# Kernel optimization log

Measured on AMD Instinct MI355X. Metric: run time of the kernel, lower is better.

Reference implementation:

```python
import jax, jax.numpy as jnp
import numpy as np

G = 4096   # num_genes
P = 4096   # num_perts
H = 64     # hidden_size
B = 4      # num_graphs
E1 = 81920 # coexpress edges
E2 = 81920 # GO edges
FF = 512   # transformer ffn
NH = 2     # attention heads
INTER, LAT = 32, 16  # VAE dims

def _bn(x, g, b, eps=1e-5):
    # BatchNorm1d in training mode: batch stats (biased var)
    m = x.mean(0); v = x.var(0)
    return (x - m) / jnp.sqrt(v + eps) * g + b

def _ln(x, g, b, eps=1e-5):
    m = x.mean(-1, keepdims=True); v = x.var(-1, keepdims=True)
    return (x - m) / jnp.sqrt(v + eps) * g + b

def _mlp2(x, w1, b1, g1, be1, w2, b2, g2, be2):
    # MLP([a,b,c]) builds Linear->BN->ReLU->Linear->BN (trailing ReLU stripped)
    h = jax.nn.relu(_bn(x @ w1.T + b1, g1, be1))
    return _bn(h @ w2.T + b2, g2, be2)

def _sgconv(x, ei, ew, w, b, n):
    # SGConv K=1: gcn_norm (self loops, symmetric norm) then linear
    src = jnp.concatenate([ei[0], jnp.arange(n)])
    dst = jnp.concatenate([ei[1], jnp.arange(n)])
    wgt = jnp.concatenate([ew, jnp.ones((n,), ew.dtype)])
    deg = jax.ops.segment_sum(wgt, dst, num_segments=n)
    dinv = jnp.where(deg > 0, 1.0 / jnp.sqrt(jnp.where(deg > 0, deg, 1.0)), 0.0)
    norm = dinv[dst] * wgt * dinv[src]
    agg = jax.ops.segment_sum(norm[:, None] * x[src], dst, num_segments=n)
    return agg @ w.T + b

def setup_inputs():
    ks = iter(jax.random.split(jax.random.key(0), 80))
    def nrm(shape, s=0.05):
        return jax.random.normal(next(ks), shape, dtype=jnp.float32) * s
    d = {}
    d['x'] = jax.random.uniform(next(ks), (B * G,), dtype=jnp.float32)
    d['pert_idx'] = jax.random.randint(next(ks), (B, 2), 0, P)
    d['mask'] = jnp.zeros((G, G), jnp.float32)
    d['ei_co'] = jax.random.randint(next(ks), (2, E1), 0, G)
    d['w_co'] = jax.random.uniform(next(ks), (E1,), dtype=jnp.float32)
    d['ei_go'] = jax.random.randint(next(ks), (2, E2), 0, P)
    d['w_go'] = jax.random.uniform(next(ks), (E2,), dtype=jnp.float32)
    d['gene_emb'] = nrm((G, H)); d['emb_pos'] = nrm((G, H)); d['pert_tbl'] = nrm((P, H))
    d['sg_co_w'] = nrm((H, H)); d['sg_co_b'] = jnp.zeros((H,))
    d['sg_go_w'] = nrm((H, H)); d['sg_go_b'] = jnp.zeros((H,))
    d['bn_emb_g'] = jnp.ones((H,)); d['bn_emb_b'] = jnp.zeros((H,))
    for pre, din, dout in [('etv2_1', H, H), ('etv2_2', H, H), ('pf_1', H, H), ('pf_2', H, H), ('rw_1', H, 2 * H), ('rw_2', 2 * H, H)]:
        d[pre + '_w'] = nrm((dout, din)); d[pre + '_b'] = jnp.zeros((dout,))
        d[pre + '_g'] = jnp.ones((dout,)); d[pre + '_be'] = jnp.zeros((dout,))
    d['bnpb_g'] = jnp.ones((H,)); d['bnpb_b'] = jnp.zeros((H,))
    d['attn_in_w'] = nrm((3 * H, H)); d['attn_in_b'] = jnp.zeros((3 * H,))
    d['attn_out_w'] = nrm((H, H)); d['attn_out_b'] = jnp.zeros((H,))
    d['ln1_g'] = jnp.ones((H,)); d['ln1_b'] = jnp.zeros((H,))
    d['ff1_w'] = nrm((FF, H)); d['ff1_b'] = jnp.zeros((FF,))
    d['ff2_w'] = nrm((H, FF)); d['ff2_b'] = jnp.zeros((H,))
    d['ln2_g'] = jnp.ones((H,)); d['ln2_b'] = jnp.zeros((H,))
    d['indv_w1'] = nrm((G, H)); d['indv_b1'] = jnp.zeros((G,))
    d['vae_e1_w'] = nrm((INTER, G)); d['vae_e1_b'] = jnp.zeros((INTER,))
    d['vae_mu_w'] = nrm((LAT, INTER)); d['vae_mu_b'] = jnp.zeros((LAT,))
    d['vae_lv_w'] = nrm((LAT, INTER)); d['vae_lv_b'] = jnp.zeros((LAT,))
    d['vae_d1_w'] = nrm((INTER, LAT)); d['vae_d1_b'] = jnp.zeros((INTER,))
    d['vae_d2_w'] = nrm((G, INTER)); d['vae_d2_b'] = jnp.zeros((G,))
    d['eps'] = jax.random.normal(next(ks), (B, LAT), dtype=jnp.float32)
    return d

def reference(x, pert_idx, mask, ei_co, w_co, ei_go, w_go, gene_emb, emb_pos, pert_tbl, sg_co_w, sg_co_b, sg_go_w, sg_go_b, bn_emb_g, bn_emb_b, etv2_1_w, etv2_1_b, etv2_1_g, etv2_1_be, etv2_2_w, etv2_2_b, etv2_2_g, etv2_2_be, pf_1_w, pf_1_b, pf_1_g, pf_1_be, pf_2_w, pf_2_b, pf_2_g, pf_2_be, rw_1_w, rw_1_b, rw_1_g, rw_1_be, rw_2_w, rw_2_b, rw_2_g, rw_2_be, bnpb_g, bnpb_b, attn_in_w, attn_in_b, attn_out_w, attn_out_b, ln1_g, ln1_b, ff1_w, ff1_b, ff2_w, ff2_b, ln2_g, ln2_b, indv_w1, indv_b1, vae_e1_w, vae_e1_b, vae_mu_w, vae_mu_b, vae_lv_w, vae_lv_b, vae_d1_w, vae_d1_b, vae_d2_w, vae_d2_b, eps):
    # gene base embedding (identical across graphs until pert fusion)
    base = jax.nn.relu(_bn(gene_emb, bn_emb_g, bn_emb_b))               # [G,H]
    pos = _sgconv(emb_pos, ei_co, w_co, sg_co_w, sg_co_b, G)            # 1 gene-GNN layer
    base = base + 0.2 * pos
    base = _mlp2(base, etv2_1_w, etv2_1_b, etv2_1_g, etv2_1_be, etv2_2_w, etv2_2_b, etv2_2_g, etv2_2_be)
    # pert embeddings propagated on GO graph
    pge = _sgconv(pert_tbl, ei_go, w_go, sg_go_w, sg_go_b, P)           # [P,H]
    # per-graph pert_track: sum of pert embeddings (all pert_idx valid)
    psum = pge[pert_idx].sum(axis=1)                                    # [B,H]
    etot = _mlp2(psum, pf_1_w, pf_1_b, pf_1_g, pf_1_be, pf_2_w, pf_2_b, pf_2_g, pf_2_be)
    base_b = base[None, :, :] + etot[:, None, :]                        # [B,G,H]
    flat = jax.nn.relu(_bn(base_b.reshape(B * G, H), bnpb_g, bnpb_b))
    out = _mlp2(flat, rw_1_w, rw_1_b, rw_1_g, rw_1_be, rw_2_w, rw_2_b, rw_2_g, rw_2_be)
    out = out.reshape(B, G, H)
    # transformer encoder layer (post-norm, relu, nhead=2), eval/no-dropout
    qkv = out @ attn_in_w.T + attn_in_b
    q, k, v = jnp.split(qkv, 3, axis=-1)
    hd = H // NH
    q = q.reshape(B, G, NH, hd); k = k.reshape(B, G, NH, hd); v = v.reshape(B, G, NH, hd)
    sc = jnp.einsum('bqhd,bkhd->bhqk', q, k) / np.float32(np.sqrt(hd)) + mask
    a = jax.nn.softmax(sc, axis=-1)
    ctx = jnp.einsum('bhqk,bkhd->bqhd', a, v).reshape(B, G, H)
    att = ctx @ attn_out_w.T + attn_out_b
    h1 = _ln(out + att, ln1_g, ln1_b)
    ff = jax.nn.relu(h1 @ ff1_w.T + ff1_b) @ ff2_w.T + ff2_b
    enc = _ln(h1 + ff, ln2_g, ln2_b)
    # per-gene linear: (enc.unsqueeze(-1)*indv_w1).sum(2)+indv_b1
    pred0 = jnp.einsum('bgh,gh->bg', enc, indv_w1) + indv_b1
    # VAE branch on raw expression
    xr = x.reshape(B, G)
    he = jax.nn.relu(xr @ vae_e1_w.T + vae_e1_b)
    mu = he @ vae_mu_w.T + vae_mu_b
    lv = he @ vae_lv_w.T + vae_lv_b
    z = mu + eps * jnp.exp(0.5 * lv)
    hdc = jax.nn.relu(z @ vae_d1_w.T + vae_d1_b)
    recon = hdc @ vae_d2_w.T + vae_d2_b
    kl = -0.5 * jnp.mean(jnp.sum(1.0 + lv - mu ** 2 - jnp.exp(lv), axis=1))
    recon = jnp.where(xr == 0, 0.0, recon)
    pred = pred0 + recon
    return (pred, kl)
```

## Files before the change

### kernel.cpp

```cpp
#include <hip/hip_runtime.h>
#include <hip/hip_bf16.h>
#include <math.h>

#define GG 4096
#define PP 4096
#define HH 64
#define BB 4
#define E1N 81920
#define E2N 81920
#define FFD 512
#define BNEPS 1e-5f
#define LOG2E 1.44269504088896341f
#define QPRE (0.17677669529663687f * LOG2E)

typedef unsigned short ushort_t;
typedef unsigned int uint_t;
using sh8 = __attribute__((ext_vector_type(8))) short;
using sh4 = __attribute__((ext_vector_type(4))) short;
using f4  = __attribute__((ext_vector_type(4))) float;

#if __has_builtin(__builtin_amdgcn_mfma_f32_16x16x16bf16_1k)
#define MFMA16(a, b, c) __builtin_amdgcn_mfma_f32_16x16x16bf16_1k((a), (b), (c), 0, 0, 0)
#elif __has_builtin(__builtin_amdgcn_mfma_f32_16x16x16_bf16)
#define MFMA16(a, b, c) __builtin_amdgcn_mfma_f32_16x16x16_bf16((a), (b), (c), 0, 0, 0)
#else
static __device__ inline f4 mfma16_asm(sh4 a, sh4 b, f4 c) {
    f4 d;
    asm volatile("v_mfma_f32_16x16x16_bf16 %0, %1, %2, %3"
                 : "=v"(d) : "v"(a), "v"(b), "v"(c));
    return d;
}
#define MFMA16(a, b, c) mfma16_asm((a), (b), (c))
#endif

#define OF_STATS   0
#define OF_DEGCO   2048
#define OF_DEGGO   6144
#define OF_PSLOT   10240
#define OF_ETOT    10752
#define OF_HDC     11008
#define OF_HE      11136
#define OF_AGGCO   12288
#define OF_BASEIN  274432
#define OF_Y1      536576
#define OF_Y2      798720
#define OF_FLAT    1060864
#define OF_RW1     2109440
#define OF_RW2     4206592
#define OF_OUT     5255168
#define OF_QKV     6303744
#define OF_H1      10498048
#define OF_QB      OF_AGGCO
#define OF_KB      (OF_AGGCO + 524288)
#define OF_VF      OF_FLAT
#define OF_OPA     OF_QKV
#define OF_OPB     OF_OUT
#define OF_LP      OF_RW1
#define OPS        1048576
#define OF_W1B     9449472
#define OF_W2B     9465856
#define OF_H1B     9482240
#define OF_FFT     OF_FLAT

__device__ inline ushort_t f2b(float f) {
    uint_t u = __builtin_bit_cast(uint_t, f);
    u += 0x7FFFu + ((u >> 16) & 1u);
    return (ushort_t)(u >> 16);
}

__device__ inline void gld16(const void* gptr, void* lptr) {
    __builtin_amdgcn_global_load_lds(
        (const __attribute__((address_space(1))) uint_t*)gptr,
        (__attribute__((address_space(3))) uint_t*)lptr, 16, 0, 0);
}

__device__ void dev_vae_he(int bid, const float* __restrict__ x, const float* __restrict__ W,
                           const float* __restrict__ bias, float* he, float* sh) {
    int b = bid >> 5, i = bid & 31;
    float s = 0.f;
    for (int g = threadIdx.x; g < 4096; g += 256) s += x[b * 4096 + g] * W[i * 4096 + g];
    sh[threadIdx.x] = s;
    __syncthreads();
    for (int o = 128; o > 0; o >>= 1) {
        if (threadIdx.x < o) sh[threadIdx.x] += sh[threadIdx.x + o];
        __syncthreads();
    }
    if (threadIdx.x == 0) he[b * 32 + i] = fmaxf(sh[0] + bias[i], 0.f);
}

__device__ void dev_vae_mid(const float* __restrict__ he,
                            const float* __restrict__ muw, const float* __restrict__ mub,
                            const float* __restrict__ lvw, const float* __restrict__ lvb,
                            const float* __restrict__ d1w, const float* __restrict__ d1b,
                            const float* __restrict__ eps, float* hdc, float* klout, float* zs) {
    int t = threadIdx.x;
    if (t < 64) {
        int b = t >> 4, l = t & 15;
        float mu = mub[l], lv = lvb[l];
        for (int i = 0; i < 32; i++) {
            float hv = he[b * 32 + i];
            mu += hv * muw[l * 32 + i];
            lv += hv * lvw[l * 32 + i];
        }
        zs[t] = mu + eps[t] * expf(0.5f * lv);
        float kterm = 1.f + lv - mu * mu - expf(lv);
        for (int o = 32; o > 0; o >>= 1) kterm += __shfl_xor(kterm, o, 64);
        if (t == 0) klout[0] = -0.5f * kterm * 0.25f;
    }
    __syncthreads();
    if (t < 128) {
        int b = t >> 5, i = t & 31;
        float a = d1b[i];
        for (int l = 0; l < 16; l++) a += zs[b * 16 + l] * d1w[i * 16 + l];
        hdc[t] = fmaxf(a, 0.f);
    }
}

__device__ void dev_edge_deg(int bid, const int* __restrict__ ei, const float* __restrict__ w,
                             float* deg, int E) {
    int e = bid * 256 + threadIdx.x;
    if (e < E) atomicAdd(&deg[ei[E + e]], w[e]);
}

__device__ void dev_cs_part(int bid, const float* __restrict__ X, int N,
                            float* sum, float* sumsq, float* sh) {
    int t = threadIdx.x;
    int col = t & 63, ro = t >> 6;
    int rows = N >> 8;
    int r0 = bid * rows;
    float s = 0.f, q = 0.f;
    for (int r = r0 + ro; r < r0 + rows; r += 4) {
        float v = X[r * 64 + col];
        s += v; q += v * v;
    }
    float* ls = sh; float* lq = sh + 256;
    ls[t] = s; lq[t] = q;
    __syncthreads();
    if (t < 64) {
        for (int j = t + 64; j < 256; j += 64) { s += ls[j]; q += lq[j]; }
        atomicAdd(&sum[t], s);
        atomicAdd(&sumsq[t], q);
    }
}

__device__ void dev_edge_agg(int bid, const int* __restrict__ ei, const float* __restrict__ w,
                             const float* __restrict__ deg, const float* __restrict__ x,
                             float* agg) {
    int gid = bid * 256 + threadIdx.x;
    int e = gid >> 6, h = gid & 63;
    if (e < E1N) {
        int src = ei[e], dst = ei[E1N + e];
        float norm = rsqrtf(deg[dst]) * w[e] * rsqrtf(deg[src]);
        atomicAdd(&agg[dst * HH + h], norm * x[src * HH + h]);
    }
}

__device__ void dev_pert_edges(int bid, const int* __restrict__ pidx, const int* __restrict__ ei,
                               const float* __restrict__ w, const float* __restrict__ deg,
                               const float* __restrict__ tbl, float* pslot) {
    int e = bid * 256 + threadIdx.x;
    if (e >= E2N) return;
    int dst = ei[E2N + e];
    int src = ei[e];
    for (int s = 0; s < 8; s++) {
        if (pidx[s] == dst) {
            float norm = rsqrtf(deg[dst]) * w[e] * rsqrtf(deg[src]);
            for (int h = 0; h < 64; h++)
                atomicAdd(&pslot[s * 64 + h], norm * tbl[src * 64 + h]);
        }
    }
}

__device__ void dev_base_combine(int bid, const float* __restrict__ gene_emb,
                                 const float* __restrict__ agg, const float* __restrict__ emb_pos,
                                 const float* __restrict__ deg,
                                 const float* __restrict__ W, const float* __restrict__ bias,
                                 const float* __restrict__ bsum, const float* __restrict__ bsq,
                                 const float* __restrict__ bg, const float* __restrict__ bb,
                                 float* out, float* sh) {
    float* Wt = sh;
    float* a = sh + 4160;
    int t = threadIdx.x;
    for (int i = t; i < 4096; i += 256) Wt[(i & 63) * 65 + (i >> 6)] = W[i];
    int rr = t >> 6, h = t & 63;
    int g = bid * 4 + rr;
    a[rr * 64 + h] = agg[g * 64 + h] + emb_pos[g * 64 + h] / deg[g];
    __syncthreads();
    float y = bias[h];
    const float* ar = a + rr * 64;
    #pragma unroll 8
    for (int k = 0; k < 64; k++) y += ar[k] * Wt[k * 65 + h];
    const float invN = 1.0f / (float)GG;
    float m = bsum[h] * invN;
    float is_ = rsqrtf(bsq[h] * invN - m * m + BNEPS);
    float v = gene_emb[g * 64 + h];
    v = (v - m) * is_ * bg[h] + bb[h];
    v = fmaxf(v, 0.f);
    out[g * 64 + h] = v + 0.2f * y;
}

__device__ void dev_pert_mlp(const float* __restrict__ pslot, const int* __restrict__ pidx,
                             const float* __restrict__ deg, const float* __restrict__ tbl,
                             const float* __restrict__ gw, const float* __restrict__ gb,
                             const float* __restrict__ w1, const float* __restrict__ b1,
                             const float* __restrict__ g1, const float* __restrict__ be1,
                             const float* __restrict__ w2, const float* __restrict__ b2,
                             const float* __restrict__ g2, const float* __restrict__ be2,
                             float* etot, float* sh) {
    float* pge = sh;
    float* psum = sh + 512;
    float* y = sh + 768;
    float* mh = sh + 1024;
    float* ih = sh + 1088;
    int t = threadIdx.x;
    for (int j = t; j < 512; j += 256) {
        int s = j >> 6, h = j & 63;
        int n = pidx[s];
        float invd = 1.0f / deg[n];
        float acc = gb[h];
        for (int k = 0; k < 64; k++)
            acc += (pslot[s * 64 + k] + tbl[n * 64 + k] * invd) * gw[h * 64 + k];
        pge[j] = acc;
    }
    __syncthreads();
    { int b = t >> 6, h = t & 63; psum[t] = pge[2 * b * 64 + h] + pge[(2 * b + 1) * 64 + h]; }
    __syncthreads();
    { int h = t & 63; int b = t >> 6;
      float acc = b1[h];
      for (int k = 0; k < 64; k++) acc += psum[b * 64 + k] * w1[h * 64 + k];
      y[t] = acc; }
    __syncthreads();
    if (t < 64) {
        float s = 0.f, sq = 0.f;
        for (int b = 0; b < 4; b++) { float v = y[b * 64 + t]; s += v; sq += v * v; }
        float m = s * 0.25f;
        mh[t] = m; ih[t] = rsqrtf(sq * 0.25f - m * m + BNEPS);
    }
    __syncthreads();
    { int h = t & 63;
      float v = (y[t] - mh[h]) * ih[h] * g1[h] + be1[h];
      psum[t] = fmaxf(v, 0.f); }
    __syncthreads();
    { int h = t & 63; int b = t >> 6;
      float acc = b2[h];
      for (int k = 0; k < 64; k++) acc += psum[b * 64 + k] * w2[h * 64 + k];
      y[t] = acc; }
    __syncthreads();
    if (t < 64) {
        float s = 0.f, sq = 0.f;
        for (int b = 0; b < 4; b++) { float v = y[b * 64 + t]; s += v; sq += v * v; }
        float m = s * 0.25f;
        mh[t] = m; ih[t] = rsqrtf(sq * 0.25f - m * m + BNEPS);
    }
    __syncthreads();
    { int h = t & 63;
      etot[t] = (y[t] - mh[h]) * ih[h] * g2[h] + be2[h]; }
}

__global__ void k_fat1(float* ws, const float* __restrict__ x,
                       const float* __restrict__ ve1_w, const float* __restrict__ ve1_b,
                       const float* __restrict__ ff1_w, const float* __restrict__ ff2_w) {
    __shared__ float sh[256];
    int bid = blockIdx.x;
    if (bid < 1024) {
        ws[OF_AGGCO + bid * 256 + threadIdx.x] = 0.f;
    } else if (bid < 1034) {
        int i = (bid - 1024) * 256 + threadIdx.x;
        if (i < 2048) ws[OF_STATS + i] = 0.f;
        else if (i < 2560) ws[OF_PSLOT + (i - 2048)] = 0.f;
    } else if (bid < 1066) {
        ws[OF_DEGCO + (bid - 1034) * 256 + threadIdx.x] = 1.0f;
    } else if (bid < 1194) {
        dev_vae_he(bid - 1066, x, ve1_w, ve1_b, ws + OF_HE, sh);
    } else {
        int i = (bid - 1194) * 256 + threadIdx.x;
        ushort_t* W1b = (ushort_t*)(ws + OF_W1B);
        ushort_t* W2b = (ushort_t*)(ws + OF_W2B);
        if (i < 32768) W1b[i] = f2b(ff1_w[i]);
        else W2b[i - 32768] = f2b(ff2_w[i - 32768]);
    }
}

__global__ void k_fat2(float* ws, const int* __restrict__ ei_co, const float* __restrict__ w_co,
                       const int* __restrict__ ei_go, const float* __restrict__ w_go,
                       const float* __restrict__ gene_emb,
                       const float* __restrict__ vmu_w, const float* __restrict__ vmu_b,
                       const float* __restrict__ vlv_w, const float* __restrict__ vlv_b,
                       const float* __restrict__ vd1_w, const float* __restrict__ vd1_b,
                       const float* __restrict__ veps, float* klout) {
    __shared__ float sh[512];
    int bid = blockIdx.x;
    if (bid < 320) dev_edge_deg(bid, ei_co, w_co, ws + OF_DEGCO, E1N);
    else if (bid < 640) dev_edge_deg(bid - 320, ei_go, w_go, ws + OF_DEGGO, E2N);
    else if (bid < 896) dev_cs_part(bid - 640, gene_emb, GG, ws + OF_STATS, ws + OF_STATS + 128, sh);
    else dev_vae_mid(ws + OF_HE, vmu_w, vmu_b, vlv_w, vlv_b, vd1_w, vd1_b, veps,
                     ws + OF_HDC, klout, sh);
}

__global__ void k_fat3(float* ws, const int* __restrict__ ei_co, const float* __restrict__ w_co,
                       const float* __restrict__ emb_pos, const int* __restrict__ pidx,
                       const int* __restrict__ ei_go, const float* __restrict__ w_go,
                       const float* __restrict__ pert_tbl) {
    int bid = blockIdx.x;
    if (bid < 20480) dev_edge_agg(bid, ei_co, w_co, ws + OF_DEGCO, emb_pos, ws + OF_AGGCO);
    else dev_pert_edges(bid - 20480, pidx, ei_go, w_go, ws + OF_DEGGO, pert_tbl, ws + OF_PSLOT);
}

__global__ void k_fat4(float* ws, const float* __restrict__ gene_emb,
                       const float* __restrict__ emb_pos,
                       const float* __restrict__ sg_co_w, const float* __restrict__ sg_co_b,
                       const float* __restrict__ bn_emb_g, const float* __restrict__ bn_emb_b,
                       const int* __restrict__ pidx, const float* __restrict__ pert_tbl,
                       const float* __restrict__ gw, const float* __restrict__ gb,
                       const float* __restrict__ w1, const float* __restrict__ b1,
                       const float* __restrict__ g1, const float* __restrict__ be1,
                       const float* __restrict__ w2, const float* __restrict__ b2,
                       const float* __restrict__ g2, const float* __restrict__ be2) {
    __shared__ float sh[4416];
    int bid = blockIdx.x;
    if (bid < 1024)
        dev_base_combine(bid, gene_emb, ws + OF_AGGCO, emb_pos, ws + OF_DEGCO,
                         sg_co_w, sg_co_b, ws + OF_STATS, ws + OF_STATS + 128,
                         bn_emb_g, bn_emb_b, ws + OF_BASEIN, sh);
    else
        dev_pert_mlp(ws + OF_PSLOT, pidx, ws + OF_DEGGO, pert_tbl, gw, gb,
                     w1, b1, g1, be1, w2, b2, g2, be2, ws + OF_ETOT, sh);
}

__launch_bounds__(256)
__global__ void k_gemm64(const float* __restrict__ X, const float* __restrict__ W,
                         const float* __restrict__ bias, float* __restrict__ Y,
                         int Cin, int Cout,
                         const float* __restrict__ bnsum, const float* __restrict__ bnsq,
                         const float* __restrict__ bng, const float* __restrict__ bnb,
                         float invN, int relu_in,
                         float* __restrict__ outsum, float* __restrict__ outsq) {
    __shared__ float Xs[64][66];
    __shared__ float Ws[64][66];
    __shared__ float bsc[64], bsh[64];
    const int t = threadIdx.x;
    const int row0 = blockIdx.x * 64, cb = blockIdx.y * 64;
    const int tx = t & 15, ty = t >> 4;
    const int c0 = tx * 4, r0 = ty * 4;
    float acc[4][4];
    #pragma unroll
    for (int j = 0; j < 4; j++)
        #pragma unroll
        for (int i = 0; i < 4; i++) acc[j][i] = 0.f;

    for (int k0 = 0; k0 < Cin; k0 += 64) {
        __syncthreads();
        if (t < 64) {
            float sc = 1.f, sh = 0.f;
            if (bnsum) {
                int c = k0 + t;
                float m = bnsum[c] * invN;
                float is_ = rsqrtf(bnsq[c] * invN - m * m + BNEPS);
                sc = is_ * bng[c]; sh = bnb[c] - m * sc;
            }
            bsc[t] = sc; bsh[t] = sh;
        }
        __syncthreads();
        for (int i = t; i < 1024; i += 256) {
            int r = i >> 4, kq = (i & 15) * 4;
            float4 v = *(const float4*)&X[(size_t)(row0 + r) * Cin + k0 + kq];
            float e0 = v.x * bsc[kq] + bsh[kq];
            float e1 = v.y * bsc[kq + 1] + bsh[kq + 1];
            float e2 = v.z * bsc[kq + 2] + bsh[kq + 2];
            float e3 = v.w * bsc[kq + 3] + bsh[kq + 3];
            if (relu_in) {
                e0 = fmaxf(e0, 0.f); e1 = fmaxf(e1, 0.f);
                e2 = fmaxf(e2, 0.f); e3 = fmaxf(e3, 0.f);
            }
            Xs[r][kq] = e0; Xs[r][kq + 1] = e1; Xs[r][kq + 2] = e2; Xs[r][kq + 3] = e3;
            float4 wv = *(const float4*)&W[(size_t)(cb + r) * Cin + k0 + kq];
            Ws[r][kq] = wv.x; Ws[r][kq + 1] = wv.y; Ws[r][kq + 2] = wv.z; Ws[r][kq + 3] = wv.w;
        }
        __syncthreads();
        #pragma unroll 4
        for (int k = 0; k < 64; k += 2) {
            float2 a[4], b[4];
            #pragma unroll
            for (int j = 0; j < 4; j++) a[j] = *(const float2*)&Xs[r0 + j][k];
            #pragma unroll
            for (int i = 0; i < 4; i++) b[i] = *(const float2*)&Ws[c0 + i][k];
            #pragma unroll
            for (int j = 0; j < 4; j++)
                #pragma unroll
                for (int i = 0; i < 4; i++)
                    acc[j][i] += a[j].x * b[i].x + a[j].y * b[i].y;
        }
    }
    float4 bi = *(const float4*)&bias[cb + c0];
    float scol[4] = {0.f, 0.f, 0.f, 0.f}, qcol[4] = {0.f, 0.f, 0.f, 0.f};
    #pragma unroll
    for (int j = 0; j < 4; j++) {
        float4 o;
        o.x = acc[j][0] + bi.x; o.y = acc[j][1] + bi.y;
        o.z = acc[j][2] + bi.z; o.w = acc[j][3] + bi.w;
        *(float4*)&Y[(size_t)(row0 + r0 + j) * Cout + cb + c0] = o;
        scol[0] += o.x; scol[1] += o.y; scol[2] += o.z; scol[3] += o.w;
        qcol[0] += o.x * o.x; qcol[1] += o.y * o.y;
        qcol[2] += o.z * o.z; qcol[3] += o.w * o.w;
    }
    if (outsum) {
        __syncthreads();
        #pragma unroll
        for (int i = 0; i < 4; i++) { Xs[ty][c0 + i] = scol[i]; Ws[ty][c0 + i] = qcol[i]; }
        __syncthreads();
        if (t < 64) {
            float ss = 0.f, qq = 0.f;
            #pragma unroll
            for (int r = 0; r < 16; r++) { ss += Xs[r][t]; qq += Ws[r][t]; }
            atomicAdd(&outsum[cb + t], ss);
            atomicAdd(&outsq[cb + t], qq);
        }
    }
}

__launch_bounds__(256)
__global__ void k_gemm_qkv(const float* __restrict__ X, const float* __restrict__ W,
                           const float* __restrict__ bias,
                           const float* __restrict__ bnsum, const float* __restrict__ bnsq,
                           const float* __restrict__ bng, const float* __restrict__ bnb,
                           ushort_t* __restrict__ Qb, ushort_t* __restrict__ Kb,
                           ushort_t* __restrict__ Vf) {
    __shared__ float Xs[64][66];
    __shared__ float Ws[64][66];
    __shared__ float bsc[64], bsh[64];
    const int t = threadIdx.x;
    const int row0 = blockIdx.x * 64, yb = blockIdx.y, cb = yb * 64;
    const int tx = t & 15, ty = t >> 4;
    const int c0 = tx * 4, r0 = ty * 4;
    const float invN = 1.0f / (float)(BB * GG);
    if (t < 64) {
        float m = bnsum[t] * invN;
        float is_ = rsqrtf(bnsq[t] * invN - m * m + BNEPS);
        float sc = is_ * bng[t];
        bsc[t] = sc; bsh[t] = bnb[t] - m * sc;
    }
    __syncthreads();
    for (int i = t; i < 1024; i += 256) {
        int r = i >> 4, kq = (i & 15) * 4;
        float4 v = *(const float4*)&X[(size_t)(row0 + r) * 64 + kq];
        Xs[r][kq] = v.x * bsc[kq] + bsh[kq];
        Xs[r][kq + 1] = v.y * bsc[kq + 1] + bsh[kq + 1];
        Xs[r][kq + 2] = v.z * bsc[kq + 2] + bsh[kq + 2];
        Xs[r][kq + 3] = v.w * bsc[kq + 3] + bsh[kq + 3];
        float4 wv = *(const float4*)&W[(size_t)(cb + r) * 64 + kq];
        Ws[r][kq] = wv.x; Ws[r][kq + 1] = wv.y; Ws[r][kq + 2] = wv.z; Ws[r][kq + 3] = wv.w;
    }
    __syncthreads();
    float acc[4][4];
    #pragma unroll
    for (int j = 0; j < 4; j++)
        #pragma unroll
        for (int i = 0; i < 4; i++) acc[j][i] = 0.f;
    #pragma unroll 4
    for (int k = 0; k < 64; k += 2) {
        float2 a[4], b[4];
        #pragma unroll
        for (int j = 0; j < 4; j++) a[j] = *(const float2*)&Xs[r0 + j][k];
        #pragma unroll
        for (int i = 0; i < 4; i++) b[i] = *(const float2*)&Ws[c0 + i][k];
        #pragma unroll
        for (int j = 0; j < 4; j++)
            #pragma unroll
            for (int i = 0; i < 4; i++)
                acc[j][i] += a[j].x * b[i].x + a[j].y * b[i].y;
    }
    float4 bi = *(const float4*)&bias[cb + c0];
    const int b2 = row0 >> 12, tile = (row0 & 4095) >> 6;
    if (yb < 2) {
        ushort_t* Dst = (yb == 0) ? Qb : Kb;
        const float sc2 = (yb == 0) ? QPRE : 1.0f;
        const int h = c0 >> 5, d = c0 & 31;
        #pragma unroll
        for (int j = 0; j < 4; j++) {
            union { ushort_t u[4]; uint2 v; } pk;
            pk.u[0] = f2b((acc[j][0] + bi.x) * sc2);
            pk.u[1] = f2b((acc[j][1] + bi.y) * sc2);
            pk.u[2] = f2b((acc[j][2] + bi.z) * sc2);
            pk.u[3] = f2b((acc[j][3] + bi.w) * sc2);
            int g = (row0 & 4095) + r0 + j;
            *(uint2*)&Dst[((size_t)(b2 * 2 + h) * GG + g) * 32 + d] = pk.v;
        }
    } else {
        __syncthreads();
        #pragma unroll
        for (int j = 0; j < 4; j++) {
            Xs[r0 + j][c0] = acc[j][0] + bi.x;
            Xs[r0 + j][c0 + 1] = acc[j][1] + bi.y;
            Xs[r0 + j][c0 + 2] = acc[j][2] + bi.z;
            Xs[r0 + j][c0 + 3] = acc[j][3] + bi.w;
        }
        __syncthreads();
        #pragma unroll
        for (int h = 0; h < 2; h++) {
            union { ushort_t u[8]; uint4 v; } pk;
            #pragma unroll
            for (int j = 0; j < 8; j++) {
                int idx = t * 8 + j;
                int g2 = idx >> 8, L = (idx >> 2) & 63, i = idx & 3;
                int key = (g2 >> 1) * 16 + ((L >> 4) << 2) + i;
                int d = ((g2 & 1) << 4) + (L & 15);
                pk.u[j] = f2b(Xs[key][h * 32 + d]);
            }
            *(uint4*)&Vf[((size_t)((b2 * 2 + h) * 64 + tile)) * 2048 + t * 8] = pk.v;
        }
    }
}

__global__ void k_flatpre(const float* __restrict__ y2, const float* __restrict__ etot,
                          const float* __restrict__ bsum, const float* __restrict__ bsq,
                          const float* __restrict__ g2, const float* __restrict__ b2,
                          float* __restrict__ out,
                          float* __restrict__ osum, float* __restrict__ osq) {
    int t = threadIdx.x;
    int h = t & 63, ro = t >> 6;
    int row0 = blockIdx.x * 64;
    const float invN = 1.0f / (float)GG;
    float m = bsum[h] * invN;
    float is_ = rsqrtf(bsq[h] * invN - m * m + BNEPS);
    float sc = is_ * g2[h];
    float sh = b2[h] - m * sc;
    float s = 0.f, q = 0.f;
    for (int r = row0 + ro; r < row0 + 64; r += 4) {
        int b = r >> 12, gh = (r & 4095) * 64 + h;
        float v = y2[gh] * sc + sh + etot[b * 64 + h];
        out[r * 64 + h] = v;
        s += v; q += v * v;
    }
    __shared__ float ls[256], lq[256];
    ls[t] = s; lq[t] = q;
    __syncthreads();
    if (t < 64) {
        s = ls[t] + ls[t + 64] + ls[t + 128] + ls[t + 192];
        q = lq[t] + lq[t + 64] + lq[t + 128] + lq[t + 192];
        atomicAdd(&osum[t], s);
        atomicAdd(&osq[t], q);
    }
}

__launch_bounds__(256)
__global__ void k_attn_mfma(const ushort_t* __restrict__ Qb, const ushort_t* __restrict__ Kb,
                            const ushort_t* __restrict__ Vf, const float* __restrict__ mask,
                            float* __restrict__ opA, float* __restrict__ opB,
                            float* __restrict__ Lp) {
    __shared__ ushort_t Kl[2][4096];
    __shared__ ushort_t Vl[2][4096];
    const int bh = blockIdx.y;
    const int split = blockIdx.z;
    const int q0 = blockIdx.x * 64;
    const int kstart = split * (GG / 4), kend = kstart + (GG / 4);
    const int t = threadIdx.x;
    const int lane = t & 63, w = t >> 6;
    const int l15 = lane & 15, quad = lane >> 4;

    const sh8 qf = *(const sh8*)&Qb[((size_t)bh * GG + q0 + w * 16 + l15) * 32 + quad * 8];
    const float* mrow = mask + (size_t)(q0 + w * 16 + l15) * GG + quad * 4;

    const size_t kfth = ((size_t)bh * GG + (t >> 6) * 16 + (t & 15)) * 32 + ((t >> 4) & 3) * 8;
    const size_t vfbh = (size_t)bh * 64;

    gld16(Kb + kfth + (size_t)kstart * 32, &Kl[0][t * 8]);
    gld16(Kb + kfth + (size_t)(kstart + 64) * 32, &Kl[0][2048 + t * 8]);
    gld16(Vf + (vfbh + (kstart >> 6)) * 2048 + t * 8, &Vl[0][t * 8]);
    gld16(Vf + (vfbh + (kstart >> 6) + 1) * 2048 + t * 8, &Vl[0][2048 + t * 8]);

    f4 O0 = {0.f, 0.f, 0.f, 0.f}, O1 = {0.f, 0.f, 0.f, 0.f};
    float ls = 0.f;

    for (int k0 = kstart; k0 < kend; k0 += 128) {
        const int cur = ((k0 - kstart) >> 7) & 1;
        __syncthreads();
        if (k0 + 128 < kend) {
            const int nxt = cur ^ 1;
            gld16(Kb + kfth + (size_t)(k0 + 128) * 32, &Kl[nxt][t * 8]);
            gld16(Kb + kfth + (size_t)(k0 + 192) * 32, &Kl[nxt][2048 + t * 8]);
            gld16(Vf + (vfbh + ((k0 + 128) >> 6)) * 2048 + t * 8, &Vl[nxt][t * 8]);
            gld16(Vf + (vfbh + ((k0 + 128) >> 6) + 1) * 2048 + t * 8, &Vl[nxt][2048 + t * 8]);
        }
        #pragma unroll
        for (int half = 0; half < 2; half++) {
            const ushort_t* Kh = &Kl[cur][half * 2048];
            const ushort_t* Vh = &Vl[cur][half * 2048];
            const int kk = k0 + half * 64;
            float4 mv[4];
            #pragma unroll
            for (int i2 = 0; i2 < 4; i2++) mv[i2] = *(const float4*)&mrow[kk + i2 * 16];
            f4 s[4];
            #pragma unroll
            for (int i2 = 0; i2 < 4; i2++) {
                sh8 kf = *(const sh8*)&Kh[(i2 * 64 + lane) * 8];
                f4 z = {0.f, 0.f, 0.f, 0.f};
                s[i2] = __builtin_amdgcn_mfma_f32_16x16x32_bf16(kf, qf, z, 0, 0, 0);
            }
            #pragma unroll
            for (int i2 = 0; i2 < 4; i2++) {
                float p0 = exp2f(fmaf(mv[i2].x, LOG2E, s[i2][0]));
                float p1 = exp2f(fmaf(mv[i2].y, LOG2E, s[i2][1]));
                float p2 = exp2f(fmaf(mv[i2].z, LOG2E, s[i2][2]));
                float p3 = exp2f(fmaf(mv[i2].w, LOG2E, s[i2][3]));
                ls += (p0 + p1) + (p2 + p3);
                union { __hip_bfloat162 h2[2]; sh4 v; } pkp;
                pkp.h2[0] = __float22bfloat162_rn(float2{p0, p1});
                pkp.h2[1] = __float22bfloat162_rn(float2{p2, p3});
                sh4 vf0 = *(const sh4*)&Vh[((i2 * 2 + 0) * 64 + lane) * 4];
                sh4 vf1 = *(const sh4*)&Vh[((i2 * 2 + 1) * 64 + lane) * 4];
                O0 = MFMA16(pkp.v, vf0, O0);
                O1 = MFMA16(pkp.v, vf1, O1);
            }
        }
    }
    ls += __shfl_xor(ls, 16, 64);
    ls += __shfl_xor(ls, 32, 64);
    float* op = (split < 3) ? (opA + (size_t)split * OPS) : opB;
    #pragma unroll
    for (int r = 0; r < 4; r++) {
        int q = q0 + w * 16 + quad * 4 + r;
        size_t o = ((size_t)bh * GG + q) * 32 + l15;
        op[o] = O0[r];
        op[o + 16] = O1[r];
    }
    if (quad == 0)
        Lp[split * 32768 + bh * GG + q0 + w * 16 + l15] = ls;
}

__global__ void k_attn_out_ln(const float* __restrict__ opA, const float* __restrict__ opB,
                              const float* __restrict__ Lp, const float* __restrict__ yrw2,
                              const float* __restrict__ W, const float* __restrict__ bias,
                              const float* __restrict__ bsum, const float* __restrict__ bsq,
                              const float* __restrict__ bg, const float* __restrict__ bb,
                              const float* __restrict__ lg, const float* __restrict__ lb,
                              float* __restrict__ h1, ushort_t* __restrict__ h1b) {
    __shared__ float Wt[64][65];
    __shared__ float Cs[16][65];
    __shared__ ushort_t Hs[16][64];
    int t = threadIdx.x;
    int row0 = blockIdx.x * 16;
    for (int i = t; i < 4096; i += 256) Wt[i & 63][i >> 6] = W[i];
    {
        int col = t & 63, rl = t >> 6;
        int hh = col >> 5, d = col & 31;
        #pragma unroll
        for (int jj = 0; jj < 4; jj++) {
            int row = row0 + rl + jj * 4;
            int b = row >> 12, q = row & 4095;
            int bhq = (b * 2 + hh) * GG + q;
            size_t oi = (size_t)bhq * 32 + d;
            float num = opA[oi] + opA[OPS + oi] + opA[2 * OPS + oi] + opB[oi];
            float den = Lp[bhq] + Lp[32768 + bhq] + Lp[65536 + bhq] + Lp[98304 + bhq];
            Cs[rl + jj * 4][col] = num / den;
        }
    }
    __syncthreads();
    int rr = t >> 6, lane = t & 63;
    const float invN = 1.0f / (float)(BB * GG);
    float m = bsum[lane] * invN;
    float is_ = rsqrtf(bsq[lane] * invN - m * m + BNEPS);
    #pragma unroll
    for (int j = 0; j < 4; j++) {
        int lrow = rr * 4 + j;
        int row = row0 + lrow;
        float acc = bias[lane];
        const float* cr = Cs[lrow];
        #pragma unroll 8
        for (int k = 0; k < 64; k++) acc += cr[k] * Wt[k][lane];
        float ov = (yrw2[row * 64 + lane] - m) * is_ * bg[lane] + bb[lane];
        float v = ov + acc;
        float s = v;
        for (int o = 32; o > 0; o >>= 1) s += __shfl_xor(s, o, 64);
        float mean = s * (1.f / 64.f);
        float d = v - mean;
        float sq = d * d;
        for (int o = 32; o > 0; o >>= 1) sq += __shfl_xor(sq, o, 64);
        float inv = rsqrtf(sq * (1.f / 64.f) + BNEPS);
        float hv = d * inv * lg[lane] + lb[lane];
        h1[row * 64 + lane] = hv;
        Hs[lrow][lane] = f2b(hv);
    }
    __syncthreads();
    if (t < 128) {
        int kt = t >> 6, lane6 = t & 63;
        int q2 = (lane6 >> 4) & 3, r15 = lane6 & 15;
        union { ushort_t u[8]; uint4 v; } pk;
        #pragma unroll
        for (int j = 0; j < 8; j++) pk.u[j] = Hs[r15][kt * 32 + q2 * 8 + j];
        *(uint4*)&h1b[((size_t)blockIdx.x * 2 + kt) * 512 + lane6 * 8] = pk.v;
    }
}

__launch_bounds__(256)
__global__ void k_ffn1(const ushort_t* __restrict__ h1b, const ushort_t* __restrict__ W1b,
                       const float* __restrict__ b1, ushort_t* __restrict__ fft) {
    __shared__ ushort_t Xl[4096];
    __shared__ ushort_t Wl[4096];
    const int t = threadIdx.x;
    const int rowblock = blockIdx.x, colblock = blockIdx.y;
    const int cb = colblock * 64;
    const int lane = t & 63, w = t >> 6;
    const int l15 = lane & 15, quad = lane >> 4;
    #pragma unroll
    for (int kt = 0; kt < 2; kt++) {
        gld16(h1b + (size_t)(((rowblock * 4 + w) * 2 + kt) * 512 + lane * 8),
              &Xl[(w * 2 + kt) * 512 + lane * 8]);
        gld16(W1b + (size_t)((cb + w * 16 + l15) * 64 + kt * 32 + quad * 8),
              &Wl[(w * 2 + kt) * 512 + lane * 8]);
    }
    __syncthreads();
    sh8 xf0 = *(const sh8*)&Xl[(w * 2 + 0) * 512 + lane * 8];
    sh8 xf1 = *(const sh8*)&Xl[(w * 2 + 1) * 512 + lane * 8];
    #pragma unroll
    for (int c = 0; c < 4; c++) {
        sh8 wf0 = *(const sh8*)&Wl[(c * 2 + 0) * 512 + lane * 8];
        sh8 wf1 = *(const sh8*)&Wl[(c * 2 + 1) * 512 + lane * 8];
        f4 z = {0.f, 0.f, 0.f, 0.f};
        f4 acc = __builtin_amdgcn_mfma_f32_16x16x32_bf16(wf0, xf0, z, 0, 0, 0);
        acc = __builtin_amdgcn_mfma_f32_16x16x32_bf16(wf1, xf1, acc, 0, 0, 0);
        float4 bv = *(const float4*)&b1[cb + c * 16 + quad * 4];
        union { ushort_t u[4]; uint2 v; } pk;
        pk.u[0] = f2b(fmaxf(acc[0] + bv.x, 0.f));
        pk.u[1] = f2b(fmaxf(acc[1] + bv.y, 0.f));
        pk.u[2] = f2b(fmaxf(acc[2] + bv.z, 0.f));
        pk.u[3] = f2b(fmaxf(acc[3] + bv.w, 0.f));
        int kt512 = colblock * 2 + (c >> 1);
        int quadp = (c & 1) * 2 + (quad >> 1);
        int j0 = (quad & 1) * 4;
        size_t o = ((size_t)(((rowblock * 4 + w) * 16 + kt512) * 64 + quadp * 16 + l15)) * 8 + j0;
        *(uint2*)&fft[o] = pk.v;
    }
}

__launch_bounds__(256)
__global__ void k_ffn2(const ushort_t* __restrict__ fft, const ushort_t* __restrict__ W2b,
                       const float* __restrict__ b2, const float* __restrict__ h1,
                       const float* __restrict__ lg, const float* __restrict__ lb,
                       const float* __restrict__ indvw, const float* __restrict__ indvb,
                       const float* __restrict__ hdc, const float* __restrict__ d2w,
                       const float* __restrict__ d2b, const float* __restrict__ x,
                       float* __restrict__ outp) {
    __shared__ ushort_t Xl[2][4096];
    __shared__ ushort_t Wl[2][4096];
    const int t = threadIdx.x;
    const int rowblock = blockIdx.x;
    const int lane = t & 63, w = t >> 6;
    const int l15 = lane & 15, quad = lane >> 4;

    #pragma unroll
    for (int kt = 0; kt < 2; kt++) {
        gld16(fft + (size_t)((((rowblock * 4 + w) * 16) + kt) * 64 + lane) * 8,
              &Xl[0][(w * 2 + kt) * 512 + lane * 8]);
        gld16(W2b + (size_t)((w * 16 + l15) * 512 + kt * 32 + quad * 8),
              &Wl[0][(w * 2 + kt) * 512 + lane * 8]);
    }
    f4 acc[4];
    #pragma unroll
    for (int c = 0; c < 4; c++) acc[c] = f4{0.f, 0.f, 0.f, 0.f};

    for (int k0 = 0; k0 < 512; k0 += 64) {
        const int cur = (k0 >> 6) & 1;
        __syncthreads();
        if (k0 + 64 < 512) {
            const int nxt = cur ^ 1;
            const int ktb = (k0 + 64) >> 5;
            #pragma unroll
            for (int kt = 0; kt < 2; kt++) {
                gld16(fft + (size_t)((((rowblock * 4 + w) * 16) + ktb + kt) * 64 + lane) * 8,
                      &Xl[nxt][(w * 2 + kt) * 512 + lane * 8]);
                gld16(W2b + (size_t)((w * 16 + l15) * 512 + k0 + 64 + kt * 32 + quad * 8),
                      &Wl[nxt][(w * 2 + kt) * 512 + lane * 8]);
            }
        }
        #pragma unroll
        for (int kt = 0; kt < 2; kt++) {
            sh8 xf = *(const sh8*)&Xl[cur][(w * 2 + kt) * 512 + lane * 8];
            #pragma unroll
            for (int c = 0; c < 4; c++) {
                sh8 wf = *(const sh8*)&Wl[cur][(c * 2 + kt) * 512 + lane * 8];
                acc[c] = __builtin_amdgcn_mfma_f32_16x16x32_bf16(wf, xf, acc[c], 0, 0, 0);
            }
        }
    }
    const int row = rowblock * 64 + w * 16 + l15;
    const int b = row >> 12, g = row & 4095;
    float v[4][4];
    float s = 0.f, sq = 0.f;
    #pragma unroll
    for (int c = 0; c < 4; c++) {
        float4 bv = *(const float4*)&b2[c * 16 + quad * 4];
        float4 hv = *(const float4*)&h1[(size_t)row * 64 + c * 16 + quad * 4];
        v[c][0] = hv.x + acc[c][0] + bv.x;
        v[c][1] = hv.y + acc[c][1] + bv.y;
        v[c][2] = hv.z + acc[c][2] + bv.z;
        v[c][3] = hv.w + acc[c][3] + bv.w;
        #pragma unroll
        for (int i = 0; i < 4; i++) { s += v[c][i]; sq += v[c][i] * v[c][i]; }
    }
    s += __shfl_xor(s, 16, 64);  s += __shfl_xor(s, 32, 64);
    sq += __shfl_xor(sq, 16, 64); sq += __shfl_xor(sq, 32, 64);
    float mean = s * (1.f / 64.f);
    float inv = rsqrtf(sq * (1.f / 64.f) - mean * mean + BNEPS);
    float pd = 0.f;
    #pragma unroll
    for (int c = 0; c < 4; c++) {
        float4 lgv = *(const float4*)&lg[c * 16 + quad * 4];
        float4 lbv = *(const float4*)&lb[c * 16 + quad * 4];
        float4 iwv = *(const float4*)&indvw[(size_t)g * 64 + c * 16 + quad * 4];
        pd += ((v[c][0] - mean) * inv * lgv.x + lbv.x) * iwv.x;
        pd += ((v[c][1] - mean) * inv * lgv.y + lbv.y) * iwv.y;
        pd += ((v[c][2] - mean) * inv * lgv.z + lbv.z) * iwv.z;
        pd += ((v[c][3] - mean) * inv * lgv.w + lbv.w) * iwv.w;
    }
    float rc = 0.f;
    #pragma unroll
    for (int i = 0; i < 8; i++)
        rc += hdc[b * 32 + quad * 8 + i] * d2w[(size_t)g * 32 + quad * 8 + i];
    pd += __shfl_xor(pd, 16, 64); pd += __shfl_xor(pd, 32, 64);
    rc += __shfl_xor(rc, 16, 64); rc += __shfl_xor(rc, 32, 64);
    if (quad == 0) {
        float recon = rc + d2b[g];
        if (x[row] == 0.f) recon = 0.f;
        outp[row] = pd + indvb[g] + recon;
    }
}

extern "C" void kernel_launch(void* const* d_in, const int* in_sizes, int n_in,
                              void* d_out, int out_size, void* d_ws, size_t ws_size,
                              hipStream_t stream) {
    const float* x        = (const float*)d_in[0];
    const int*   pert_idx = (const int*)  d_in[1];
    const float* mask     = (const float*)d_in[2];
    const int*   ei_co    = (const int*)  d_in[3];
    const float* w_co     = (const float*)d_in[4];
    const int*   ei_go    = (const int*)  d_in[5];
    const float* w_go     = (const float*)d_in[6];
    const float* gene_emb = (const float*)d_in[7];
    const float* emb_pos  = (const float*)d_in[8];
    const float* pert_tbl = (const float*)d_in[9];
    const float* sg_co_w  = (const float*)d_in[10];
    const float* sg_co_b  = (const float*)d_in[11];
    const float* sg_go_w  = (const float*)d_in[12];
    const float* sg_go_b  = (const float*)d_in[13];
    const float* bn_emb_g = (const float*)d_in[14];
    const float* bn_emb_b = (const float*)d_in[15];
    const float* etv1_w   = (const float*)d_in[16];
    const float* etv1_b   = (const float*)d_in[17];
    const float* etv1_g   = (const float*)d_in[18];
    const float* etv1_be  = (const float*)d_in[19];
    const float* etv2_w   = (const float*)d_in[20];
    const float* etv2_b   = (const float*)d_in[21];
    const float* etv2_g   = (const float*)d_in[22];
    const float* etv2_be  = (const float*)d_in[23];
    const float* pf1_w    = (const float*)d_in[24];
    const float* pf1_b    = (const float*)d_in[25];
    const float* pf1_g    = (const float*)d_in[26];
    const float* pf1_be   = (const float*)d_in[27];
    const float* pf2_w    = (const float*)d_in[28];
    const float* pf2_b    = (const float*)d_in[29];
    const float* pf2_g    = (const float*)d_in[30];
    const float* pf2_be   = (const float*)d_in[31];
    const float* rw1_w    = (const float*)d_in[32];
    const float* rw1_b    = (const float*)d_in[33];
    const float* rw1_g    = (const float*)d_in[34];
    const float* rw1_be   = (const float*)d_in[35];
    const float* rw2_w    = (const float*)d_in[36];
    const float* rw2_b    = (const float*)d_in[37];
    const float* rw2_g    = (const float*)d_in[38];
    const float* rw2_be   = (const float*)d_in[39];
    const float* bnpb_g   = (const float*)d_in[40];
    const float* bnpb_b   = (const float*)d_in[41];
    const float* ain_w    = (const float*)d_in[42];
    const float* ain_b    = (const float*)d_in[43];
    const float* aout_w   = (const float*)d_in[44];
    const float* aout_b   = (const float*)d_in[45];
    const float* ln1_g    = (const float*)d_in[46];
    const float* ln1_b    = (const float*)d_in[47];
    const float* ff1_w    = (const float*)d_in[48];
    const float* ff1_b    = (const float*)d_in[49];
    const float* ff2_w    = (const float*)d_in[50];
    const float* ff2_b    = (const float*)d_in[51];
    const float* ln2_g    = (const float*)d_in[52];
    const float* ln2_b    = (const float*)d_in[53];
    const float* indv_w   = (const float*)d_in[54];
    const float* indv_b   = (const float*)d_in[55];
    const float* ve1_w    = (const float*)d_in[56];
    const float* ve1_b    = (const float*)d_in[57];
    const float* vmu_w    = (const float*)d_in[58];
    const float* vmu_b    = (const float*)d_in[59];
    const float* vlv_w    = (const float*)d_in[60];
    const float* vlv_b    = (const float*)d_in[61];
    const float* vd1_w    = (const float*)d_in[62];
    const float* vd1_b    = (const float*)d_in[63];
    const float* vd2_w    = (const float*)d_in[64];
    const float* vd2_b    = (const float*)d_in[65];
    const float* veps     = (const float*)d_in[66];

    float* ws   = (float*)d_ws;
    float* outp = (float*)d_out;

    float* stm1 = ws + OF_STATS + 1 * 256; float* sti1 = stm1 + 128;
    float* stm2 = ws + OF_STATS + 2 * 256; float* sti2 = stm2 + 128;
    float* stm3 = ws + OF_STATS + 3 * 256; float* sti3 = stm3 + 128;
    float* stm4 = ws + OF_STATS + 4 * 256; float* sti4 = stm4 + 128;
    float* stm5 = ws + OF_STATS + 5 * 256; float* sti5 = stm5 + 128;

    float* basein = ws + OF_BASEIN;
    float* y1     = ws + OF_Y1;
    float* y2     = ws + OF_Y2;
    float* flat   = ws + OF_FLAT;
    float* yrw1   = ws + OF_RW1;
    float* yrw2   = ws + OF_RW2;
    float* h1     = ws + OF_H1;
    float* opA    = ws + OF_OPA;
    float* opB    = ws + OF_OPB;
    float* Lp     = ws + OF_LP;
    ushort_t* Qb  = (ushort_t*)(ws + OF_QB);
    ushort_t* Kb  = (ushort_t*)(ws + OF_KB);
    ushort_t* Vf  = (ushort_t*)(ws + OF_VF);
    ushort_t* W1b = (ushort_t*)(ws + OF_W1B);
    ushort_t* W2b = (ushort_t*)(ws + OF_W2B);
    ushort_t* h1b = (ushort_t*)(ws + OF_H1B);
    ushort_t* fft = (ushort_t*)(ws + OF_FFT);

    const int NG = BB * GG;
    const float iG = 1.0f / (float)GG, iNG = 1.0f / (float)NG;

    k_fat1<<<1450, 256, 0, stream>>>(ws, x, ve1_w, ve1_b, ff1_w, ff2_w);
    k_fat2<<<897, 256, 0, stream>>>(ws, ei_co, w_co, ei_go, w_go, gene_emb,
                                    vmu_w, vmu_b, vlv_w, vlv_b, vd1_w, vd1_b,
                                    veps, outp + NG);
    k_fat3<<<20800, 256, 0, stream>>>(ws, ei_co, w_co, emb_pos, pert_idx,
                                      ei_go, w_go, pert_tbl);
    k_fat4<<<1025, 256, 0, stream>>>(ws, gene_emb, emb_pos, sg_co_w, sg_co_b,
                                     bn_emb_g, bn_emb_b, pert_idx, pert_tbl,
                                     sg_go_w, sg_go_b,
                                     pf1_w, pf1_b, pf1_g, pf1_be,
                                     pf2_w, pf2_b, pf2_g, pf2_be);
    k_gemm64<<<dim3(GG / 64, 1), 256, 0, stream>>>(basein, etv1_w, etv1_b, y1, 64, 64,
                                                   nullptr, nullptr, nullptr, nullptr, 0.f, 0,
                                                   stm1, sti1);
    k_gemm64<<<dim3(GG / 64, 1), 256, 0, stream>>>(y1, etv2_w, etv2_b, y2, 64, 64,
                                                   stm1, sti1, etv1_g, etv1_be, iG, 1,
                                                   stm2, sti2);
    k_flatpre<<<NG / 64, 256, 0, stream>>>(y2, ws + OF_ETOT, stm2, sti2, etv2_g, etv2_be,
                                           flat, stm3, sti3);
    k_gemm64<<<dim3(NG / 64, 2), 256, 0, stream>>>(flat, rw1_w, rw1_b, yrw1, 64, 128,
                                                   stm3, sti3, bnpb_g, bnpb_b, iNG, 1,
                                                   stm4, sti4);
    k_gemm64<<<dim3(NG / 64, 1), 256, 0, stream>>>(yrw1, rw2_w, rw2_b, yrw2, 128, 64,
                                                   stm4, sti4, rw1_g, rw1_be, iNG, 1,
                                                   stm5, sti5);
    k_gemm_qkv<<<dim3(NG / 64, 3), 256, 0, stream>>>(yrw2, ain_w, ain_b,
                                                     stm5, sti5, rw2_g, rw2_be,
                                                     Qb, Kb, Vf);
    k_attn_mfma<<<dim3(GG / 64, BB * 2, 4), 256, 0, stream>>>(Qb, Kb, Vf, mask,
                                                              opA, opB, Lp);
    k_attn_out_ln<<<NG / 16, 256, 0, stream>>>(opA, opB, Lp, yrw2, aout_w, aout_b,
                                               stm5, sti5, rw2_g, rw2_be,
                                               ln1_g, ln1_b, h1, h1b);
    k_ffn1<<<dim3(NG / 64, FFD / 64), 256, 0, stream>>>(h1b, W1b, ff1_b, fft);
    k_ffn2<<<NG / 64, 256, 0, stream>>>(fft, W2b, ff2_b, h1, ln2_g, ln2_b,
                                        indv_w, indv_b, ws + OF_HDC, vd2_w, vd2_b,
                                        x, outp);
}
```

Measured before the change: 521.9 us.

## Process all batch-heads per attention block to reuse mask loads across heads

```diff
diff --git a/kernel.cpp b/kernel.cpp
--- a/kernel.cpp
+++ b/kernel.cpp
@@ -261,19 +261,23 @@
                        const float* __restrict__ ve1_w, const float* __restrict__ ve1_b,
                        const float* __restrict__ ff1_w, const float* __restrict__ ff2_w) {
     __shared__ float sh[256];
+    const float4 z4 = {0.f, 0.f, 0.f, 0.f};
+    const float4 o4 = {1.f, 1.f, 1.f, 1.f};
     int bid = blockIdx.x;
-    if (bid < 1024) {
-        ws[OF_AGGCO + bid * 256 + threadIdx.x] = 0.f;
-    } else if (bid < 1034) {
-        int i = (bid - 1024) * 256 + threadIdx.x;
-        if (i < 2048) ws[OF_STATS + i] = 0.f;
-        else if (i < 2560) ws[OF_PSLOT + (i - 2048)] = 0.f;
-    } else if (bid < 1066) {
-        ws[OF_DEGCO + (bid - 1034) * 256 + threadIdx.x] = 1.0f;
-    } else if (bid < 1194) {
-        dev_vae_he(bid - 1066, x, ve1_w, ve1_b, ws + OF_HE, sh);
+    if (bid < 256) {
+        int i = bid * 256 + threadIdx.x;
+        *(float4*)&ws[OF_AGGCO + i * 4] = z4;
+    } else if (bid < 259) {
+        int i = (bid - 256) * 256 + threadIdx.x;
+        if (i < 512) *(float4*)&ws[OF_STATS + i * 4] = z4;
+        else if (i < 640) *(float4*)&ws[OF_PSLOT + (i - 512) * 4] = z4;
+    } else if (bid < 267) {
+        int i = (bid - 259) * 256 + threadIdx.x;
+        *(float4*)&ws[OF_DEGCO + i * 4] = o4;
+    } else if (bid < 395) {
+        dev_vae_he(bid - 267, x, ve1_w, ve1_b, ws + OF_HE, sh);
     } else {
-        int i = (bid - 1194) * 256 + threadIdx.x;
+        int i = (bid - 395) * 256 + threadIdx.x;
         ushort_t* W1b = (ushort_t*)(ws + OF_W1B);
         ushort_t* W2b = (ushort_t*)(ws + OF_W2B);
         if (i < 32768) W1b[i] = f2b(ff1_w[i]);
@@ -542,89 +546,130 @@
     }
 }
 
-__launch_bounds__(256)
+__launch_bounds__(512)
 __global__ void k_attn_mfma(const ushort_t* __restrict__ Qb, const ushort_t* __restrict__ Kb,
                             const ushort_t* __restrict__ Vf, const float* __restrict__ mask,
                             float* __restrict__ opA, float* __restrict__ opB,
                             float* __restrict__ Lp) {
-    __shared__ ushort_t Kl[2][4096];
-    __shared__ ushort_t Vl[2][4096];
-    const int bh = blockIdx.y;
-    const int split = blockIdx.z;
+    __shared__ ushort_t Kl[2][8][2048];
+    __shared__ ushort_t Vl[2][8][2048];
+    const int split = blockIdx.y;
     const int q0 = blockIdx.x * 64;
     const int kstart = split * (GG / 4), kend = kstart + (GG / 4);
     const int t = threadIdx.x;
     const int lane = t & 63, w = t >> 6;
+    const int qg = w >> 1, kh = w & 1;
     const int l15 = lane & 15, quad = lane >> 4;
-
-    const sh8 qf = *(const sh8*)&Qb[((size_t)bh * GG + q0 + w * 16 + l15) * 32 + quad * 8];
-    const float* mrow = mask + (size_t)(q0 + w * 16 + l15) * GG + quad * 4;
-
-    const size_t kfth = ((size_t)bh * GG + (t >> 6) * 16 + (t & 15)) * 32 + ((t >> 4) & 3) * 8;
-    const size_t vfbh = (size_t)bh * 64;
-
-    gld16(Kb + kfth + (size_t)kstart * 32, &Kl[0][t * 8]);
-    gld16(Kb + kfth + (size_t)(kstart + 64) * 32, &Kl[0][2048 + t * 8]);
-    gld16(Vf + (vfbh + (kstart >> 6)) * 2048 + t * 8, &Vl[0][t * 8]);
-    gld16(Vf + (vfbh + (kstart >> 6) + 1) * 2048 + t * 8, &Vl[0][2048 + t * 8]);
-
-    f4 O0 = {0.f, 0.f, 0.f, 0.f}, O1 = {0.f, 0.f, 0.f, 0.f};
-    float ls = 0.f;
-
-    for (int k0 = kstart; k0 < kend; k0 += 128) {
-        const int cur = ((k0 - kstart) >> 7) & 1;
+    const int i2a = kh * 2, i2b = kh * 2 + 1;
+
+    sh8 qf[8];
+    #pragma unroll
+    for (int bh = 0; bh < 8; bh++)
+        qf[bh] = *(const sh8*)&Qb[((size_t)bh * GG + q0 + qg * 16 + l15) * 32 + quad * 8];
+    const float* mrow = mask + (size_t)(q0 + qg * 16 + l15) * GG + quad * 4;
+
+    auto stage = [&](int buf, int k0) {
+        #pragma unroll
+        for (int s = 0; s < 4; s++) {
+            int idx = s * 512 + t;
+            int bh = idx >> 8, c = idx & 255;
+            int key = ((c >> 6) << 4) + (c & 15);
+            int chunk = (c >> 4) & 3;
+            gld16(Kb + ((size_t)bh * GG + k0 + key) * 32 + chunk * 8, &Kl[buf][bh][c * 8]);
+            gld16(Vf + ((size_t)(bh * 64 + (k0 >> 6))) * 2048 + c * 8, &Vl[buf][bh][c * 8]);
+        }
+    };
+    stage(0, kstart);
+
+    f4 O0[8], O1[8];
+    float ls[8];
+    #pragma unroll
+    for (int bh = 0; bh < 8; bh++) {
+        O0[bh] = f4{0.f, 0.f, 0.f, 0.f};
+        O1[bh] = f4{0.f, 0.f, 0.f, 0.f};
+        ls[bh] = 0.f;
+    }
+
+    for (int k0 = kstart; k0 < kend; k0 += 64) {
+        const int cur = ((k0 - kstart) >> 6) & 1;
         __syncthreads();
-        if (k0 + 128 < kend) {
-            const int nxt = cur ^ 1;
-            gld16(Kb + kfth + (size_t)(k0 + 128) * 32, &Kl[nxt][t * 8]);
-            gld16(Kb + kfth + (size_t)(k0 + 192) * 32, &Kl[nxt][2048 + t * 8]);
-            gld16(Vf + (vfbh + ((k0 + 128) >> 6)) * 2048 + t * 8, &Vl[nxt][t * 8]);
-            gld16(Vf + (vfbh + ((k0 + 128) >> 6) + 1) * 2048 + t * 8, &Vl[nxt][2048 + t * 8]);
-        }
-        #pragma unroll
-        for (int half = 0; half < 2; half++) {
-            const ushort_t* Kh = &Kl[cur][half * 2048];
-            const ushort_t* Vh = &Vl[cur][half * 2048];
-            const int kk = k0 + half * 64;
-            float4 mv[4];
-            #pragma unroll
-            for (int i2 = 0; i2 < 4; i2++) mv[i2] = *(const float4*)&mrow[kk + i2 * 16];
-            f4 s[4];
-            #pragma unroll
-            for (int i2 = 0; i2 < 4; i2++) {
-                sh8 kf = *(const sh8*)&Kh[(i2 * 64 + lane) * 8];
-                f4 z = {0.f, 0.f, 0.f, 0.f};
-                s[i2] = __builtin_amdgcn_mfma_f32_16x16x32_bf16(kf, qf, z, 0, 0, 0);
-            }
-            #pragma unroll
-            for (int i2 = 0; i2 < 4; i2++) {
-                float p0 = exp2f(fmaf(mv[i2].x, LOG2E, s[i2][0]));
-                float p1 = exp2f(fmaf(mv[i2].y, LOG2E, s[i2][1]));
-                float p2 = exp2f(fmaf(mv[i2].z, LOG2E, s[i2][2]));
-                float p3 = exp2f(fmaf(mv[i2].w, LOG2E, s[i2][3]));
-                ls += (p0 + p1) + (p2 + p3);
+        if (k0 + 64 < kend) stage(cur ^ 1, k0 + 64);
+        float4 mva = *(const float4*)&mrow[k0 + i2a * 16];
+        float4 mvb = *(const float4*)&mrow[k0 + i2b * 16];
+        #pragma unroll
+        for (int bh = 0; bh < 8; bh++) {
+            sh8 kfa = *(const sh8*)&Kl[cur][bh][(i2a * 64 + lane) * 8];
+            sh8 kfb = *(const sh8*)&Kl[cur][bh][(i2b * 64 + lane) * 8];
+            f4 z = {0.f, 0.f, 0.f, 0.f};
+            f4 sa = __builtin_amdgcn_mfma_f32_16x16x32_bf16(kfa, qf[bh], z, 0, 0, 0);
+            f4 sb = __builtin_amdgcn_mfma_f32_16x16x32_bf16(kfb, qf[bh], z, 0, 0, 0);
+            {
+                float p0 = exp2f(fmaf(mva.x, LOG2E, sa[0]));
+                float p1 = exp2f(fmaf(mva.y, LOG2E, sa[1]));
+                float p2 = exp2f(fmaf(mva.z, LOG2E, sa[2]));
+                float p3 = exp2f(fmaf(mva.w, LOG2E, sa[3]));
+                ls[bh] += (p0 + p1) + (p2 + p3);
                 union { __hip_bfloat162 h2[2]; sh4 v; } pkp;
                 pkp.h2[0] = __float22bfloat162_rn(float2{p0, p1});
                 pkp.h2[1] = __float22bfloat162_rn(float2{p2, p3});
-                sh4 vf0 = *(const sh4*)&Vh[((i2 * 2 + 0) * 64 + lane) * 4];
-                sh4 vf1 = *(const sh4*)&Vh[((i2 * 2 + 1) * 64 + lane) * 4];
-                O0 = MFMA16(pkp.v, vf0, O0);
-                O1 = MFMA16(pkp.v, vf1, O1);
+                sh4 vf0 = *(const sh4*)&Vl[cur][bh][((i2a * 2 + 0) * 64 + lane) * 4];
+                sh4 vf1 = *(const sh4*)&Vl[cur][bh][((i2a * 2 + 1) * 64 + lane) * 4];
+                O0[bh] = MFMA16(pkp.v, vf0, O0[bh]);
+                O1[bh] = MFMA16(pkp.v, vf1, O1[bh]);
             }
-        }
-    }
-    ls += __shfl_xor(ls, 16, 64);
-    ls += __shfl_xor(ls, 32, 64);
-    float* op = (split < 3) ? (opA + (size_t)split * OPS) : opB;
-    #pragma unroll
-    for (int r = 0; r < 4; r++) {
-        int q = q0 + w * 16 + quad * 4 + r;
-        size_t o = ((size_t)bh * GG + q) * 32 + l15;
-        op[o] = O0[r];
-        op[o + 16] = O1[r];
-    }
-    if (quad == 0)
-        Lp[split * 32768 + bh * GG + q0 + w * 16 + l15] = ls;
+            {
+                float p0 = exp2f(fmaf(mvb.x, LOG2E, sb[0]));
+                float p1 = exp2f(fmaf(mvb.y, LOG2E, sb[1]));
+                float p2 = exp2f(fmaf(mvb.z, LOG2E, sb[2]));
+                float p3 = exp2f(fmaf(mvb.w, LOG2E, sb[3]));
+                ls[bh] += (p0 + p1) + (p2 + p3);
+                union { __hip_bfloat162 h2[2]; sh4 v; } pkp;
+                pkp.h2[0] = __float22bfloat162_rn(float2{p0, p1});
+                pkp.h2[1] = __float22bfloat162_rn(float2{p2, p3});
+                sh4 vf0 = *(const sh4*)&Vl[cur][bh][((i2b * 2 + 0) * 64 + lane) * 4];
+                sh4 vf1 = *(const sh4*)&Vl[cur][bh][((i2b * 2 + 1) * 64 + lane) * 4];
+                O0[bh] = MFMA16(pkp.v, vf0, O0[bh]);
+                O1[bh] = MFMA16(pkp.v, vf1, O1[bh]);
+            }
+        }
+    }
+    #pragma unroll
+    for (int bh = 0; bh < 8; bh++) {
+        ls[bh] += __shfl_xor(ls[bh], 16, 64);
+        ls[bh] += __shfl_xor(ls[bh], 32, 64);
+    }
+    __syncthreads();
+    float* Ox = (float*)&Kl[0][0][0];
+    float* Lx = (float*)&Vl[0][0][0];
+    if (kh == 0) {
+        #pragma unroll
+        for (int bh = 0; bh < 8; bh++) {
+            #pragma unroll
+            for (int r = 0; r < 4; r++) {
+                int ql = qg * 16 + quad * 4 + r;
+                Ox[(bh * 64 + ql) * 32 + l15] = O0[bh][r];
+                Ox[(bh * 64 + ql) * 32 + l15 + 16] = O1[bh][r];
+            }
+            if (quad == 0) Lx[bh * 64 + qg * 16 + l15] = ls[bh];
+        }
+    }
+    __syncthreads();
+    if (kh == 1) {
+        float* op = (split < 3) ? (opA + (size_t)split * OPS) : opB;
+        #pragma unroll
+        for (int bh = 0; bh < 8; bh++) {
+            #pragma unroll
+            for (int r = 0; r < 4; r++) {
+                int ql = qg * 16 + quad * 4 + r;
+                size_t o = ((size_t)bh * GG + q0 + ql) * 32 + l15;
+                op[o] = O0[bh][r] + Ox[(bh * 64 + ql) * 32 + l15];
+                op[o + 16] = O1[bh][r] + Ox[(bh * 64 + ql) * 32 + l15 + 16];
+            }
+            if (quad == 0)
+                Lp[split * 32768 + bh * GG + q0 + qg * 16 + l15] =
+                    ls[bh] + Lx[bh * 64 + qg * 16 + l15];
+        }
+    }
 }
 
 __global__ void k_attn_out_ln(const float* __restrict__ opA, const float* __restrict__ opB,
@@ -926,7 +971,7 @@
     const int NG = BB * GG;
     const float iG = 1.0f / (float)GG, iNG = 1.0f / (float)NG;
 
-    k_fat1<<<1450, 256, 0, stream>>>(ws, x, ve1_w, ve1_b, ff1_w, ff2_w);
+    k_fat1<<<651, 256, 0, stream>>>(ws, x, ve1_w, ve1_b, ff1_w, ff2_w);
     k_fat2<<<897, 256, 0, stream>>>(ws, ei_co, w_co, ei_go, w_go, gene_emb,
                                     vmu_w, vmu_b, vlv_w, vlv_b, vd1_w, vd1_b,
                                     veps, outp + NG);
@@ -954,8 +999,7 @@
     k_gemm_qkv<<<dim3(NG / 64, 3), 256, 0, stream>>>(yrw2, ain_w, ain_b,
                                                      stm5, sti5, rw2_g, rw2_be,
                                                      Qb, Kb, Vf);
-    k_attn_mfma<<<dim3(GG / 64, BB * 2, 4), 256, 0, stream>>>(Qb, Kb, Vf, mask,
-                                                              opA, opB, Lp);
+    k_attn_mfma<<<dim3(GG / 64, 4), 512, 0, stream>>>(Qb, Kb, Vf, mask, opA, opB, Lp);
     k_attn_out_ln<<<NG / 16, 256, 0, stream>>>(opA, opB, Lp, yrw2, aout_w, aout_b,
                                                stm5, sti5, rw2_g, rw2_be,
                                                ln1_g, ln1_b, h1, h1b);
```

Measured after the change: 527.1 us. No clear change (+1.0%).
